# Kernel tuning notes

Hardware: AMD Instinct MI355X
Metric: run time of the kernel (lower is better)

Reference implementation:

```python
import jax, jax.numpy as jnp
import numpy as np

N = 500_000      # total rows (e.g. video frames)
S = 10_000       # number of segments (shots)
D_IN = 128
D_OUT = 128


def setup_inputs() -> dict:
    key = jax.random.key(0)
    k1, k2, k3 = jax.random.split(key, 3)
    inp = jax.random.normal(k1, (N, D_IN), dtype=jnp.float32)
    # contiguous non-overlapping segments covering [0, N): graph[j] = (start_j, end_j) inclusive
    rng = np.random.default_rng(0)
    cuts = np.sort(rng.choice(np.arange(1, N), size=S - 1, replace=False))
    starts = np.concatenate([[0], cuts]).astype(np.int64)
    ends = np.concatenate([cuts - 1, [N - 1]]).astype(np.int64)
    graph = jnp.asarray(np.stack([starts, ends], axis=1))  # [S, 2]
    # nn.Linear params (kaiming-uniform-ish scale is irrelevant for correctness baseline)
    W = jax.random.normal(k2, (D_OUT, D_IN), dtype=jnp.float32) * (1.0 / np.sqrt(D_IN))
    b = jax.random.normal(k3, (D_OUT,), dtype=jnp.float32) * 0.01
    return {"input": inp, "graph": graph, "W": W, "b": b}


def reference(input, graph, W, b):
    # One big GEMM for the projection (instead of per-segment Linear calls) ...
    y = input @ W.T + b                              # [N, D_OUT]
    n = input.shape[0]
    s = graph.shape[0]
    starts = graph[:, 0]
    ends = graph[:, 1]
    rows = jnp.arange(n)
    # ... then a single irregular segment reduction over ragged boundaries.
    seg_id = jnp.clip(jnp.searchsorted(starts, rows, side="right") - 1, 0, s - 1)  # [N]
    valid = (rows >= starts[seg_id]) & (rows <= ends[seg_id])  # guards any uncovered rows
    y = jnp.where(valid[:, None], y, 0.0)
    return jax.ops.segment_sum(y, seg_id, num_segments=s)     # [S, D_OUT]
```

## Files before the change

kernel.cpp:

```cpp
#include <hip/hip_runtime.h>
#include <hip/hip_bf16.h>


#define D 128
#define D4 32

__device__ __forceinline__ void f4add(float4& a, const float4& v) {
  a.x += v.x; a.y += v.y; a.z += v.z; a.w += v.w;
}

__global__ __launch_bounds__(256) void seg_sum_kernel(
    const float* __restrict__ in, const int* __restrict__ graph,
    float* __restrict__ Xs, int N, int S) {
  int s   = blockIdx.x;
  int tid = threadIdx.x;
  int rg  = tid >> 5;
  int c4  = tid & 31;

  int rs  = graph[2 * s];
  int re  = graph[2 * s + 1];
  int nxt = (s + 1 < S) ? (graph[2 * s + 2] - 1) : (N - 1);
  re = min(re, min(nxt, N - 1));
  rs = max(rs, 0);
  int cnt = max(0, re - rs + 1);

  const float4* p = (const float4*)in + (size_t)rs * D4 + c4;
  float4 a0 = make_float4(0.f, 0.f, 0.f, 0.f);
  float4 a1 = make_float4(0.f, 0.f, 0.f, 0.f);

  int r = rg;
  for (; r + 8 < cnt; r += 16) {
    float4 v0 = p[r * D4];
    float4 v1 = p[(r + 8) * D4];
    f4add(a0, v0);
    f4add(a1, v1);
  }
  for (; r < cnt; r += 8) {
    float4 v0 = p[r * D4];
    f4add(a0, v0);
  }
  f4add(a0, a1);

  __shared__ float4 red[256];
  red[tid] = a0;
  __syncthreads();
  if (tid < 128) { f4add(red[tid], red[tid + 128]); }
  __syncthreads();
  if (tid < 64)  { f4add(red[tid], red[tid + 64]); }
  __syncthreads();
  if (tid < 32) {
    float4 r4 = red[tid];
    f4add(r4, red[tid + 32]);
    ((float4*)Xs)[s * D4 + tid] = r4;
  }
}

#define SEG_PB 16
#define OUT_PB 64
#define WT_STRIDE 65

__global__ __launch_bounds__(256) void seg_gemm_kernel(
    const float* __restrict__ Xs, const float* __restrict__ W,
    const float* __restrict__ b, const int* __restrict__ graph,
    float* __restrict__ out, int N, int S) {
  __shared__ float Wt[D * WT_STRIDE];
  __shared__ __align__(16) float XsL[SEG_PB * D];
  __shared__ float cntL[SEG_PB];

  int tid   = threadIdx.x;
  int s0    = blockIdx.x * SEG_PB;
  int oBase = blockIdx.y * OUT_PB;

  #pragma unroll
  for (int rnd = 0; rnd < 8; ++rnd) {
    int linear = rnd * 256 + tid;
    int op     = linear >> 5;
    int d4     = (linear & 31) << 2;
    float4 w = *(const float4*)(W + (oBase + op) * D + d4);
    Wt[(d4 + 0) * WT_STRIDE + op] = w.x;
    Wt[(d4 + 1) * WT_STRIDE + op] = w.y;
    Wt[(d4 + 2) * WT_STRIDE + op] = w.z;
    Wt[(d4 + 3) * WT_STRIDE + op] = w.w;
  }
  {
    const float4* src = (const float4*)(Xs + s0 * D);
    float4* dst = (float4*)XsL;
    dst[tid]       = src[tid];
    dst[tid + 256] = src[tid + 256];
  }
  if (tid < SEG_PB) {
    int s   = s0 + tid;
    int rs  = graph[2 * s];
    int re  = graph[2 * s + 1];
    int nxt = (s + 1 < S) ? (graph[2 * s + 2] - 1) : (N - 1);
    re = min(re, min(nxt, N - 1));
    rs = max(rs, 0);
    cntL[tid] = (float)max(0, re - rs + 1);
  }
  __syncthreads();

  int op = tid & 63;
  int g  = tid >> 6;
  float acc[4] = {0.f, 0.f, 0.f, 0.f};

  const float4* xs4 = (const float4*)XsL;
  #pragma unroll 8
  for (int d4 = 0; d4 < D4; ++d4) {
    float w0 = Wt[(4 * d4 + 0) * WT_STRIDE + op];
    float w1 = Wt[(4 * d4 + 1) * WT_STRIDE + op];
    float w2 = Wt[(4 * d4 + 2) * WT_STRIDE + op];
    float w3 = Wt[(4 * d4 + 3) * WT_STRIDE + op];
    #pragma unroll
    for (int j = 0; j < 4; ++j) {
      float4 x = xs4[(4 * j + g) * D4 + d4];
      acc[j] += x.x * w0 + x.y * w1 + x.z * w2 + x.w * w3;
    }
  }

  float bo = b[oBase + op];
  #pragma unroll
  for (int j = 0; j < 4; ++j) {
    int sl = 4 * j + g;
    out[(s0 + sl) * D + oBase + op] = acc[j] + cntL[sl] * bo;
  }
}

extern "C" void kernel_launch(void* const* d_in, const int* in_sizes, int n_in,
                              void* d_out, int out_size, void* d_ws, size_t ws_size,
                              hipStream_t stream) {
  const float* in    = (const float*)d_in[0];
  const int*   graph = (const int*)d_in[1];
  const float* W     = (const float*)d_in[2];
  const float* b     = (const float*)d_in[3];
  float* out = (float*)d_out;

  const int N = in_sizes[0] / D;
  const int S = in_sizes[1] / 2;

  float* Xs = (float*)d_ws;

  seg_sum_kernel<<<S, 256, 0, stream>>>(in, graph, Xs, N, S);

  dim3 grid2(S / SEG_PB, D / OUT_PB);
  seg_gemm_kernel<<<grid2, 256, 0, stream>>>(Xs, W, b, graph, out, N, S);
}
```

Before: 370.7 us.

## Split segment reduction into fixed row chunks with atomic merging of boundary segments

```diff
diff --git a/kernel.cpp b/kernel.cpp
--- a/kernel.cpp
+++ b/kernel.cpp
@@ -4,54 +4,92 @@
 
 #define D 128
 #define D4 32
+#define CHUNK 256
 
 __device__ __forceinline__ void f4add(float4& a, const float4& v) {
   a.x += v.x; a.y += v.y; a.z += v.z; a.w += v.w;
 }
 
-__global__ __launch_bounds__(256) void seg_sum_kernel(
+__global__ __launch_bounds__(256) void zero_xs_kernel(float4* Xs4, int n4) {
+  int i = blockIdx.x * 256 + threadIdx.x;
+  if (i < n4) Xs4[i] = make_float4(0.f, 0.f, 0.f, 0.f);
+}
+
+__global__ __launch_bounds__(256) void seg_sum_chunk_kernel(
     const float* __restrict__ in, const int* __restrict__ graph,
     float* __restrict__ Xs, int N, int S) {
-  int s   = blockIdx.x;
   int tid = threadIdx.x;
+  int c4  = tid & 31;
   int rg  = tid >> 5;
-  int c4  = tid & 31;
 
-  int rs  = graph[2 * s];
-  int re  = graph[2 * s + 1];
-  int nxt = (s + 1 < S) ? (graph[2 * s + 2] - 1) : (N - 1);
-  re = min(re, min(nxt, N - 1));
-  rs = max(rs, 0);
-  int cnt = max(0, re - rs + 1);
+  int row0   = blockIdx.x * CHUNK;
+  int rowEnd = min(row0 + CHUNK, N) - 1;
+  if (row0 > rowEnd) return;
 
-  const float4* p = (const float4*)in + (size_t)rs * D4 + c4;
-  float4 a0 = make_float4(0.f, 0.f, 0.f, 0.f);
-  float4 a1 = make_float4(0.f, 0.f, 0.f, 0.f);
+  int lo = 0, hi = S - 1;
+  while (lo < hi) {
+    int mid = (lo + hi + 1) >> 1;
+    if (graph[2 * mid] <= row0) lo = mid; else hi = mid - 1;
+  }
 
-  int r = rg;
-  for (; r + 8 < cnt; r += 16) {
-    float4 v0 = p[r * D4];
-    float4 v1 = p[(r + 8) * D4];
-    f4add(a0, v0);
-    f4add(a1, v1);
-  }
-  for (; r < cnt; r += 8) {
-    float4 v0 = p[r * D4];
-    f4add(a0, v0);
-  }
-  f4add(a0, a1);
+  __shared__ float4 buf[2][3][32];
+  const float4* in4 = (const float4*)in;
+  int parity = 0;
 
-  __shared__ float4 red[256];
-  red[tid] = a0;
-  __syncthreads();
-  if (tid < 128) { f4add(red[tid], red[tid + 128]); }
-  __syncthreads();
-  if (tid < 64)  { f4add(red[tid], red[tid + 64]); }
-  __syncthreads();
-  if (tid < 32) {
-    float4 r4 = red[tid];
-    f4add(r4, red[tid + 32]);
-    ((float4*)Xs)[s * D4 + tid] = r4;
+  int s = lo;
+  while (true) {
+    int rs    = graph[2 * s];
+    int reRaw = graph[2 * s + 1];
+    int nxt   = (s + 1 < S) ? graph[2 * s + 2] : N;
+    int re    = min(reRaw, min(nxt - 1, N - 1));
+    int rs_c  = max(rs, 0);
+    int a     = max(rs_c, row0);
+    int b2    = min(re, rowEnd);
+
+    if (a <= b2) {
+      int len = b2 - a + 1;
+      const float4* p = in4 + (size_t)a * D4 + c4;
+      float4 acc0 = make_float4(0.f, 0.f, 0.f, 0.f);
+      float4 acc1 = make_float4(0.f, 0.f, 0.f, 0.f);
+      int r = rg;
+      for (; r + 8 < len; r += 16) {
+        float4 v0 = p[(size_t)r * D4];
+        float4 v1 = p[(size_t)(r + 8) * D4];
+        f4add(acc0, v0);
+        f4add(acc1, v1);
+      }
+      for (; r < len; r += 8) f4add(acc0, p[(size_t)r * D4]);
+      f4add(acc0, acc1);
+
+      float4 o;
+      o.x = __shfl_xor(acc0.x, 32, 64);
+      o.y = __shfl_xor(acc0.y, 32, 64);
+      o.z = __shfl_xor(acc0.z, 32, 64);
+      o.w = __shfl_xor(acc0.w, 32, 64);
+      f4add(acc0, o);
+
+      int wv = tid >> 6;
+      if ((tid & 32) == 0 && wv > 0) buf[parity][wv - 1][c4] = acc0;
+      __syncthreads();
+      if (tid < 32) {
+        f4add(acc0, buf[parity][0][c4]);
+        f4add(acc0, buf[parity][1][c4]);
+        f4add(acc0, buf[parity][2][c4]);
+        bool full = (rs_c >= row0) && (re <= rowEnd);
+        if (full) {
+          ((float4*)Xs)[(size_t)s * D4 + c4] = acc0;
+        } else {
+          float* q = Xs + (size_t)s * D + c4 * 4;
+          atomicAdd(q + 0, acc0.x);
+          atomicAdd(q + 1, acc0.y);
+          atomicAdd(q + 2, acc0.z);
+          atomicAdd(q + 3, acc0.w);
+        }
+      }
+      parity ^= 1;
+    }
+    if (s + 1 >= S || graph[2 * s + 2] > rowEnd) break;
+    ++s;
   }
 }
 
@@ -139,7 +177,11 @@
 
   float* Xs = (float*)d_ws;
 
-  seg_sum_kernel<<<S, 256, 0, stream>>>(in, graph, Xs, N, S);
+  int n4 = S * D4;
+  zero_xs_kernel<<<(n4 + 255) / 256, 256, 0, stream>>>((float4*)Xs, n4);
+
+  int nBlocks = (N + CHUNK - 1) / CHUNK;
+  seg_sum_chunk_kernel<<<nBlocks, 256, 0, stream>>>(in, graph, Xs, N, S);
 
   dim3 grid2(S / SEG_PB, D / OUT_PB);
   seg_gemm_kernel<<<grid2, 256, 0, stream>>>(Xs, W, b, graph, out, N, S);
```

New measurement: 377.0 us. Within noise of the previous version (+1.7%).
